# Kernel tuning notes

Measured on AMD Instinct MI355X. Metric: run time of the kernel, lower is better.

Reference implementation:

```python
import jax, jax.numpy as jnp
import numpy as np

HEAD_DIM = 64
NUM_Q_HEADS = 16
NUM_KV_HEADS = 4
MIN_TS = 1.0
MAX_TS = 10000.0


def _timescale(d):
    frac = 2.0 * jnp.arange(d // 2, dtype=jnp.float32) / d
    return MIN_TS * (MAX_TS / MIN_TS) ** frac  # [d/2]


def _rope(v, pos):
    # v: [B,S,H,D] float, pos: [B,S] int
    ts = _timescale(v.shape[-1])
    sinu = pos[:, :, None, None].astype(jnp.float32) / ts  # [B,S,1,D/2]
    sin, cos = jnp.sin(sinu), jnp.cos(sinu)
    x1, x2 = jnp.split(v.astype(jnp.float32), 2, axis=-1)
    return jnp.concatenate([x1 * cos - x2 * sin, x2 * cos + x1 * sin], axis=-1)


def setup_inputs() -> dict:
    key = jax.random.key(0)
    ks = jax.random.split(key, 5)
    B, S, E = 2, 2048, 1024
    Hq, Hk, D = NUM_Q_HEADS, NUM_KV_HEADS, HEAD_DIM
    sc = 0.02
    x = jax.random.normal(ks[0], (B, S, E), dtype=jnp.float32)
    q_pos = jnp.broadcast_to(jnp.arange(S, dtype=jnp.int32), (B, S))
    Wq = jax.random.normal(ks[1], (E, Hq * D), dtype=jnp.float32) * sc
    Wk = jax.random.normal(ks[2], (E, Hk * D), dtype=jnp.float32) * sc
    Wv = jax.random.normal(ks[3], (E, Hk * D), dtype=jnp.float32) * sc
    Wo = jax.random.normal(ks[4], (Hq * D, E), dtype=jnp.float32) * sc
    return {"x": x, "q_pos": q_pos, "Wq": Wq, "Wk": Wk, "Wv": Wv, "Wo": Wo}


def reference(x, q_pos, Wq, Wk, Wv, Wo):
    B, S, E = x.shape
    Hq, Hk, D = NUM_Q_HEADS, NUM_KV_HEADS, HEAD_DIM
    G = Hq // Hk  # gqa groups

    q = (x @ Wq).reshape(B, S, Hq, D)
    k = (x @ Wk).reshape(B, S, Hk, D)
    v = (x @ Wv).reshape(B, S, Hk, D)

    q = _rope(q, q_pos)  # kv_pos defaults to q_pos
    k = _rope(k, q_pos)

    # [B,Hk,G,S,D] grouped query heads vs shared kv heads
    qg = q.transpose(0, 2, 1, 3).reshape(B, Hk, G, S, D)
    kt = k.transpose(0, 2, 1, 3)  # [B,Hk,S,D]
    vt = v.transpose(0, 2, 1, 3)

    # NOTE: original uses scale=1.0 (no 1/sqrt(D))
    scores = jnp.einsum('bhgqd,bhkd->bhgqk', qg, kt)
    probs = jax.nn.softmax(scores, axis=-1)
    out = jnp.einsum('bhgqk,bhkd->bhgqd', probs, vt)  # [B,Hk,G,S,D]
    out = out.reshape(B, Hq, S, D).transpose(0, 2, 1, 3).reshape(B, S, Hq * D)
    return out @ Wo
```

## Files before the change

### kernel.cpp

```cpp
#include <hip/hip_runtime.h>
#include <hip/hip_fp16.h>
#include <math.h>

typedef __attribute__((ext_vector_type(8))) _Float16 half8;
typedef __attribute__((ext_vector_type(4))) _Float16 half4;
typedef __attribute__((ext_vector_type(4))) float f32x4;
typedef __attribute__((ext_vector_type(16))) float f32x16;
typedef __attribute__((ext_vector_type(4))) unsigned uint4v;

#define HQ 16
#define HK 4
#define DH 64
#define NB 2
#define SEQ 2048
#define EDIM 1024
#define KD 1024

__device__ __forceinline__ void gload16(const void* g, void* l) {
  __builtin_amdgcn_global_load_lds(
      (const __attribute__((address_space(1))) void*)g,
      (__attribute__((address_space(3))) void*)l, 16, 0, 0);
}

__global__ __launch_bounds__(256) void prep_cvt_rope(
    const float* __restrict__ x, _Float16* __restrict__ xh,
    const int* __restrict__ qpos, float2* __restrict__ tab) {
  int bx = blockIdx.x;
  int tid = threadIdx.x;
  if (bx < 4096) {
    int i = bx * 256 + tid;
    float4 v = ((const float4*)x)[i];
    half4 h;
    h[0] = (_Float16)v.x; h[1] = (_Float16)v.y; h[2] = (_Float16)v.z; h[3] = (_Float16)v.w;
    *(half4*)(xh + (size_t)i * 4) = h;
  } else {
    int i = (bx - 4096) * 256 + tid;
    int row = i >> 5, d = i & 31;
    float ang = (float)qpos[row] * expf((float)d * -0.2878231366242558f);
    float sn, cs;
    sincosf(ang, &sn, &cs);
    tab[i] = make_float2(sn, cs);
  }
}

__global__ __launch_bounds__(256) void transpose_w4(
    const float* __restrict__ Wq, const float* __restrict__ Wk,
    const float* __restrict__ Wv, const float* __restrict__ Wo,
    _Float16* __restrict__ WT, _Float16* __restrict__ WoT) {
  int z = blockIdx.z;
  const float* W;
  _Float16* dst;
  int N, roff;
  if (z == 0)      { W = Wq; N = 1024; roff = 0;    dst = WT; }
  else if (z == 1) { W = Wk; N = 256;  roff = 1024; dst = WT;  if (blockIdx.x >= 4) return; }
  else if (z == 2) { W = Wv; N = 256;  roff = 1280; dst = WT;  if (blockIdx.x >= 4) return; }
  else             { W = Wo; N = 1024; roff = 0;    dst = WoT; }

  __shared__ float t[64][65];
  int n0 = blockIdx.x * 64, k0 = blockIdx.y * 64;
  int tid = threadIdx.x;
#pragma unroll
  for (int p = 0; p < 4; ++p) {
    int idx = tid + p * 256;
    int r = idx >> 4;
    int c4 = idx & 15;
    float4 v = *(const float4*)(W + (size_t)(k0 + r) * N + n0 + c4 * 4);
    t[r][c4 * 4 + 0] = v.x; t[r][c4 * 4 + 1] = v.y;
    t[r][c4 * 4 + 2] = v.z; t[r][c4 * 4 + 3] = v.w;
  }
  __syncthreads();
#pragma unroll
  for (int p = 0; p < 4; ++p) {
    int idx = tid + p * 256;
    int n = idx >> 4;
    int k4 = idx & 15;
    half4 h;
    h[0] = (_Float16)t[k4 * 4 + 0][n]; h[1] = (_Float16)t[k4 * 4 + 1][n];
    h[2] = (_Float16)t[k4 * 4 + 2][n]; h[3] = (_Float16)t[k4 * 4 + 3][n];
    *(half4*)(dst + (size_t)(roff + n0 + n) * KD + k0 + k4 * 4) = h;
  }
}

__global__ __launch_bounds__(256) void transpose_v_kernel(const _Float16* __restrict__ vhp,
                                                          _Float16* __restrict__ vtp) {
  __shared__ _Float16 t[64][72];
  int bh = blockIdx.y;
  int s0 = blockIdx.x * 64;
  const _Float16* src = vhp + ((size_t)bh * SEQ + s0) * DH;
  _Float16* dst = vtp + (size_t)bh * DH * SEQ + s0;
  int tid = threadIdx.x;
#pragma unroll
  for (int p = 0; p < 2; ++p) {
    int idx = tid + p * 256;
    int r = idx >> 3, c8 = idx & 7;
    half8 v = *(const half8*)(src + (size_t)r * DH + c8 * 8);
#pragma unroll
    for (int i = 0; i < 8; ++i) t[r][c8 * 8 + i] = v[i];
  }
  __syncthreads();
#pragma unroll
  for (int p = 0; p < 2; ++p) {
    int idx = tid + p * 256;
    int d = idx >> 3, c8 = idx & 7;
    half8 v;
#pragma unroll
    for (int i = 0; i < 8; ++i) v[i] = t[c8 * 8 + i][d];
    *(half8*)(dst + (size_t)d * SEQ + c8 * 8) = v;
  }
}

#define SWZ(r, kb) ((kb) ^ (((r) & 7) << 4))

__global__ __launch_bounds__(256) void gemm_qkv_rope(
    const _Float16* __restrict__ xh, const _Float16* __restrict__ WT,
    const float2* __restrict__ rtab,
    _Float16* __restrict__ qh, _Float16* __restrict__ kh, _Float16* __restrict__ vh) {
  __shared__ char As[64 * 64 * 2];
  __shared__ char Bs[128 * 64 * 2];
  int tid = threadIdx.x, lane = tid & 63, wid = tid >> 6;
  int wr = wid >> 1, wc = wid & 1;
  int bm = blockIdx.x, bn = blockIdx.y;

  const char* Ag = (const char*)(xh + (size_t)bm * 64 * KD);
  const char* Bg = (const char*)(WT + (size_t)bn * 128 * KD);

  int colS = 16 * ((lane & 7) ^ (lane >> 3));
  int rS = (lane >> 3);

  f32x4 acc[2][4] = {};

  for (int kt = 0; kt < KD / 64; ++kt) {
#pragma unroll
    for (int p = 0; p < 2; ++p) {
      int sb = wid * 2 + p;
      int r = sb * 8 + rS;
      gload16(Ag + (size_t)r * (KD * 2) + kt * 128 + colS, As + sb * 1024);
    }
#pragma unroll
    for (int p = 0; p < 4; ++p) {
      int sb = wid * 4 + p;
      int r = sb * 8 + rS;
      gload16(Bg + (size_t)r * (KD * 2) + kt * 128 + colS, Bs + sb * 1024);
    }
    __syncthreads();
#pragma unroll
    for (int kk = 0; kk < 2; ++kk) {
      int kb = kk * 64 + (lane >> 4) * 16;
      half8 af[2], bf[4];
#pragma unroll
      for (int mf = 0; mf < 2; ++mf) {
        int r = wr * 32 + mf * 16 + (lane & 15);
        af[mf] = *(const half8*)(As + r * 128 + SWZ(r, kb));
      }
#pragma unroll
      for (int nf = 0; nf < 4; ++nf) {
        int r = wc * 64 + nf * 16 + (lane & 15);
        bf[nf] = *(const half8*)(Bs + r * 128 + SWZ(r, kb));
      }
#pragma unroll
      for (int mf = 0; mf < 2; ++mf)
#pragma unroll
        for (int nf = 0; nf < 4; ++nf)
          acc[mf][nf] = __builtin_amdgcn_mfma_f32_16x16x32_f16(af[mf], bf[nf], acc[mf][nf], 0, 0, 0);
    }
    __syncthreads();
  }

  int col0 = bn * 128 + wc * 64;
  int row_base = bm * 64 + wr * 32;
#pragma unroll
  for (int mf = 0; mf < 2; ++mf) {
#pragma unroll
    for (int j = 0; j < 4; ++j) {
      int row = row_base + mf * 16 + (lane >> 4) * 4 + j;
      int b = row >> 11, s = row & (SEQ - 1);
      if (col0 < 1024) {
        int hq = col0 >> 6;
        size_t base = (((size_t)b * HQ + hq) * SEQ + s) * DH;
#pragma unroll
        for (int nf = 0; nf < 2; ++nf) {
          int d = nf * 16 + (lane & 15);
          float2 scv = rtab[row * 32 + d];
          float x1 = acc[mf][nf][j], x2 = acc[mf][nf + 2][j];
          qh[base + d]      = (_Float16)(x1 * scv.y - x2 * scv.x);
          qh[base + d + 32] = (_Float16)(x2 * scv.y + x1 * scv.x);
        }
      } else if (col0 < 1280) {
        int hk = (col0 - 1024) >> 6;
        size_t base = (((size_t)b * HK + hk) * SEQ + s) * DH;
#pragma unroll
        for (int nf = 0; nf < 2; ++nf) {
          int d = nf * 16 + (lane & 15);
          float2 scv = rtab[row * 32 + d];
          float x1 = acc[mf][nf][j], x2 = acc[mf][nf + 2][j];
          kh[base + d]      = (_Float16)(x1 * scv.y - x2 * scv.x);
          kh[base + d + 32] = (_Float16)(x2 * scv.y + x1 * scv.x);
        }
      } else {
        int hk = (col0 - 1280) >> 6;
        size_t base = (((size_t)b * HK + hk) * SEQ + s) * DH;
#pragma unroll
        for (int nf = 0; nf < 4; ++nf) {
          int d = nf * 16 + (lane & 15);
          vh[base + d] = (_Float16)acc[mf][nf][j];
        }
      }
    }
  }
}

__global__ __launch_bounds__(256) void attn_kernel(
    const _Float16* __restrict__ qh, const _Float16* __restrict__ kh,
    const _Float16* __restrict__ vt, _Float16* __restrict__ oh) {
  __shared__ char Ks[128 * 64 * 2];
  __shared__ char Vs[64 * 128 * 2];

  int tid = threadIdx.x, lane = tid & 63, wid = tid >> 6;
  int half = lane >> 5, l31 = lane & 31;
  bool lopart = (half == 0);
  int qt = blockIdx.x, bh = blockIdx.y;
  int b = bh >> 4, hq = bh & 15, hk = hq >> 2;

  const _Float16* Qg = qh + (((size_t)b * HQ + hq) * SEQ + qt * 128 + wid * 32 + l31) * DH;
  const char* Kg = (const char*)(kh + (((size_t)b * HK + hk) * SEQ) * DH);
  const char* Vtg = (const char*)(vt + (size_t)(b * HK + hk) * DH * SEQ);

  const _Float16 l2e = (_Float16)1.44269504f;
  half8 qf[4];
#pragma unroll
  for (int ks = 0; ks < 4; ++ks) {
    half8 q0 = *(const half8*)(Qg + ks * 16 + half * 8);
#pragma unroll
    for (int i = 0; i < 8; ++i) q0[i] = q0[i] * l2e;
    qf[ks] = q0;
  }

  int colK = 16 * ((lane & 7) ^ (lane >> 3));
  int rK = lane >> 3;

  f32x16 oacc[2] = {};
  float m = -3e38f, l = 0.f;

  for (int kt = 0; kt < SEQ / 128; ++kt) {
#pragma unroll
    for (int p = 0; p < 4; ++p) {
      int r = (wid * 4 + p) * 8 + rK;
      gload16(Kg + (size_t)(kt * 128 + r) * 128 + colK, Ks + (wid * 4 + p) * 1024);
      int d = (wid * 4 + p) * 4 + (lane >> 4);
      int colV = ((lane & 15) * 16) ^ ((d & 7) << 4);
      gload16(Vtg + (size_t)d * (SEQ * 2) + kt * 256 + colV, Vs + (wid * 4 + p) * 1024);
    }
    __syncthreads();

    f32x16 sacc[4] = {};
    __builtin_amdgcn_s_setprio(1);
#pragma unroll
    for (int b4 = 0; b4 < 4; ++b4) {
      int r = b4 * 32 + l31;
#pragma unroll
      for (int ks = 0; ks < 4; ++ks) {
        half8 kf = *(const half8*)(Ks + r * 128 + SWZ(r, ks * 32 + half * 16));
        sacc[b4] = __builtin_amdgcn_mfma_f32_32x32x16_f16(kf, qf[ks], sacc[b4], 0, 0, 0);
      }
    }
    __builtin_amdgcn_s_setprio(0);

    float pmb[4];
#pragma unroll
    for (int b4 = 0; b4 < 4; ++b4) {
      f32x16 v = sacc[b4];
      float a0 = fmaxf(v[0], v[1]),   a1 = fmaxf(v[2], v[3]);
      float a2 = fmaxf(v[4], v[5]),   a3 = fmaxf(v[6], v[7]);
      float a4 = fmaxf(v[8], v[9]),   a5 = fmaxf(v[10], v[11]);
      float a6 = fmaxf(v[12], v[13]), a7 = fmaxf(v[14], v[15]);
      float b0 = fmaxf(a0, a1), b1 = fmaxf(a2, a3);
      float b2 = fmaxf(a4, a5), b3 = fmaxf(a6, a7);
      pmb[b4] = fmaxf(fmaxf(b0, b1), fmaxf(b2, b3));
    }
    float pm = fmaxf(fmaxf(pmb[0], pmb[1]), fmaxf(pmb[2], pmb[3]));
    pm = fmaxf(pm, __shfl_xor(pm, 32, 64));
    float mnew = fmaxf(m, pm);
    float alpha = __builtin_amdgcn_exp2f(m - mnew);
    m = mnew;
    oacc[0] *= alpha;
    oacc[1] *= alpha;
    l *= alpha;
    float ps0 = 0.f, ps1 = 0.f, ps2 = 0.f, ps3 = 0.f;

#pragma unroll
    for (int b4 = 0; b4 < 4; ++b4) {
      float e[16];
#pragma unroll
      for (int r = 0; r < 4; ++r)  { e[r] = __builtin_amdgcn_exp2f(sacc[b4][r] - m);  ps0 += e[r]; }
#pragma unroll
      for (int r = 4; r < 8; ++r)  { e[r] = __builtin_amdgcn_exp2f(sacc[b4][r] - m);  ps1 += e[r]; }
#pragma unroll
      for (int r = 8; r < 12; ++r) { e[r] = __builtin_amdgcn_exp2f(sacc[b4][r] - m);  ps2 += e[r]; }
#pragma unroll
      for (int r = 12; r < 16; ++r){ e[r] = __builtin_amdgcn_exp2f(sacc[b4][r] - m);  ps3 += e[r]; }
      unsigned W0[4], W1[4];
#pragma unroll
      for (int qd = 0; qd < 4; ++qd) {
        W0[qd] = __builtin_bit_cast(unsigned, __builtin_amdgcn_cvt_pkrtz(e[4 * qd + 0], e[4 * qd + 1]));
        W1[qd] = __builtin_bit_cast(unsigned, __builtin_amdgcn_cvt_pkrtz(e[4 * qd + 2], e[4 * qd + 3]));
      }
      half8 pf[2];
#pragma unroll
      for (int s = 0; s < 2; ++s) {
        unsigned selA = lopart ? W0[2 * s + 1] : W0[2 * s];
        unsigned crA = (unsigned)__shfl_xor((int)selA, 32, 64);
        unsigned selB = lopart ? W1[2 * s + 1] : W1[2 * s];
        unsigned crB = (unsigned)__shfl_xor((int)selB, 32, 64);
        uint4v u;
        u[0] = lopart ? W0[2 * s] : crA;
        u[1] = lopart ? W1[2 * s] : crB;
        u[2] = lopart ? crA : W0[2 * s + 1];
        u[3] = lopart ? crB : W1[2 * s + 1];
        pf[s] = __builtin_bit_cast(half8, u);
      }
      __builtin_amdgcn_s_setprio(1);
#pragma unroll
      for (int s = 0; s < 2; ++s) {
        int kvb = b4 * 64 + s * 32 + half * 16;
#pragma unroll
        for (int dblk = 0; dblk < 2; ++dblk) {
          int d = dblk * 32 + l31;
          half8 vf = *(const half8*)(Vs + d * 256 + SWZ(d, kvb));
          oacc[dblk] = __builtin_amdgcn_mfma_f32_32x32x16_f16(vf, pf[s], oacc[dblk], 0, 0, 0);
        }
      }
      __builtin_amdgcn_s_setprio(0);
    }
    float ps = (ps0 + ps1) + (ps2 + ps3);
    ps += __shfl_xor(ps, 32, 64);
    l += ps;
    __syncthreads();
  }

  int s = qt * 128 + wid * 32 + l31;
  float invl = 1.f / l;
  size_t base = ((size_t)b * SEQ + s) * 1024 + hq * 64;
#pragma unroll
  for (int dblk = 0; dblk < 2; ++dblk) {
#pragma unroll
    for (int qd = 0; qd < 4; ++qd) {
      half4 o;
#pragma unroll
      for (int j = 0; j < 4; ++j) o[j] = (_Float16)(oacc[dblk][qd * 4 + j] * invl);
      *(half4*)(oh + base + dblk * 32 + qd * 8 + half * 4) = o;
    }
  }
}

__global__ __launch_bounds__(256) void gemm_out(
    const _Float16* __restrict__ ah, const _Float16* __restrict__ WoT,
    float* __restrict__ out) {
  __shared__ char As[64 * 64 * 2];
  __shared__ char Bs[128 * 64 * 2];
  int tid = threadIdx.x, lane = tid & 63, wid = tid >> 6;
  int wr = wid >> 1, wc = wid & 1;
  int bm = blockIdx.x, bn = blockIdx.y;
  const char* Ag = (const char*)(ah + (size_t)bm * 64 * KD);
  const char* Bg = (const char*)(WoT + (size_t)bn * 128 * KD);
  int colS = 16 * ((lane & 7) ^ (lane >> 3));
  int rS = (lane >> 3);
  f32x4 acc[2][4] = {};

  for (int kt = 0; kt < KD / 64; ++kt) {
#pragma unroll
    for (int p = 0; p < 2; ++p) {
      int sb = wid * 2 + p;
      int r = sb * 8 + rS;
      gload16(Ag + (size_t)r * (KD * 2) + kt * 128 + colS, As + sb * 1024);
    }
#pragma unroll
    for (int p = 0; p < 4; ++p) {
      int sb = wid * 4 + p;
      int r = sb * 8 + rS;
      gload16(Bg + (size_t)r * (KD * 2) + kt * 128 + colS, Bs + sb * 1024);
    }
    __syncthreads();
#pragma unroll
    for (int kk = 0; kk < 2; ++kk) {
      int kb = kk * 64 + (lane >> 4) * 16;
      half8 af[2], bf[4];
#pragma unroll
      for (int mf = 0; mf < 2; ++mf) {
        int r = wr * 32 + mf * 16 + (lane & 15);
        af[mf] = *(const half8*)(As + r * 128 + SWZ(r, kb));
      }
#pragma unroll
      for (int nf = 0; nf < 4; ++nf) {
        int r = wc * 64 + nf * 16 + (lane & 15);
        bf[nf] = *(const half8*)(Bs + r * 128 + SWZ(r, kb));
      }
#pragma unroll
      for (int mf = 0; mf < 2; ++mf)
#pragma unroll
        for (int nf = 0; nf < 4; ++nf)
          acc[mf][nf] = __builtin_amdgcn_mfma_f32_16x16x32_f16(af[mf], bf[nf], acc[mf][nf], 0, 0, 0);
    }
    __syncthreads();
  }

  int row0 = bm * 64 + wr * 32, col0 = bn * 128 + wc * 64;
#pragma unroll
  for (int mf = 0; mf < 2; ++mf)
#pragma unroll
    for (int j = 0; j < 4; ++j) {
      int row = row0 + mf * 16 + (lane >> 4) * 4 + j;
#pragma unroll
      for (int nf = 0; nf < 4; ++nf)
        out[(size_t)row * 1024 + col0 + nf * 16 + (lane & 15)] = acc[mf][nf][j];
    }
}

extern "C" void kernel_launch(void* const* d_in, const int* in_sizes, int n_in,
                              void* d_out, int out_size, void* d_ws, size_t ws_size,
                              hipStream_t stream) {
  const float* x  = (const float*)d_in[0];
  const int* qpos = (const int*)d_in[1];
  const float* Wq = (const float*)d_in[2];
  const float* Wk = (const float*)d_in[3];
  const float* Wv = (const float*)d_in[4];
  const float* Wo = (const float*)d_in[5];
  float* out = (float*)d_out;

  char* ws = (char*)d_ws;
  _Float16* xh  = (_Float16*)(ws);
  _Float16* WT  = (_Float16*)(ws + 8388608);
  _Float16* WoT = (_Float16*)(ws + 11534336);
  _Float16* qhp = (_Float16*)(ws + 13631488);
  _Float16* khp = (_Float16*)(ws + 22020096);
  _Float16* vhp = (_Float16*)(ws + 24117248);
  _Float16* ohp = (_Float16*)(ws + 26214400);
  float2*   rtab = (float2*)(ws + 34603008);
  _Float16* vtp = (_Float16*)(ws + 35651584);

  prep_cvt_rope<<<4608, 256, 0, stream>>>(x, xh, qpos, rtab);
  transpose_w4<<<dim3(16, 16, 4), 256, 0, stream>>>(Wq, Wk, Wv, Wo, WT, WoT);
  gemm_qkv_rope<<<dim3(64, 12), 256, 0, stream>>>(xh, WT, rtab, qhp, khp, vhp);
  transpose_v_kernel<<<dim3(32, 8), 256, 0, stream>>>(vhp, vtp);
  attn_kernel<<<dim3(16, 32), 256, 0, stream>>>(qhp, khp, vtp, ohp);
  gemm_out<<<dim3(64, 8), 256, 0, stream>>>(ohp, WoT, out);
}
```

Baseline: 110.0 us.

## Use lazy softmax rescale, MFMA row sums, and permlane32 swap in attention

The attention inner loop now rescales the running output only when some lane's new max exceeds the old max by more than 8 in log2 units, so most tiles skip the alpha multiply. The row-sum of probabilities is computed with an extra MFMA against a vector of ones instead of scalar adds plus a cross-lane shuffle. The lane-half exchange of packed probabilities uses v_permlane32_swap in place of a shuffle with selects, and the max reduction is reorganized into three-operand form. These changes cut VALU work in the softmax at the cost of one more MFMA per sub-block, and the lazy rescale lets probabilities exceed 1 before conversion to fp16, which risks precision loss or overflow.

```diff
diff --git a/kernel.cpp b/kernel.cpp
--- a/kernel.cpp
+++ b/kernel.cpp
@@ -217,7 +217,6 @@
 
   int tid = threadIdx.x, lane = tid & 63, wid = tid >> 6;
   int half = lane >> 5, l31 = lane & 31;
-  bool lopart = (half == 0);
   int qt = blockIdx.x, bh = blockIdx.y;
   int b = bh >> 4, hq = bh & 15, hk = hq >> 2;
 
@@ -234,12 +233,16 @@
     for (int i = 0; i < 8; ++i) q0[i] = q0[i] * l2e;
     qf[ks] = q0;
   }
+  half8 ones;
+#pragma unroll
+  for (int i = 0; i < 8; ++i) ones[i] = (_Float16)1.f;
 
   int colK = 16 * ((lane & 7) ^ (lane >> 3));
   int rK = lane >> 3;
 
   f32x16 oacc[2] = {};
-  float m = -3e38f, l = 0.f;
+  f32x16 psacc = {};
+  float m = -3e38f;
 
   for (int kt = 0; kt < SEQ / 128; ++kt) {
 #pragma unroll
@@ -269,35 +272,31 @@
 #pragma unroll
     for (int b4 = 0; b4 < 4; ++b4) {
       f32x16 v = sacc[b4];
-      float a0 = fmaxf(v[0], v[1]),   a1 = fmaxf(v[2], v[3]);
-      float a2 = fmaxf(v[4], v[5]),   a3 = fmaxf(v[6], v[7]);
-      float a4 = fmaxf(v[8], v[9]),   a5 = fmaxf(v[10], v[11]);
-      float a6 = fmaxf(v[12], v[13]), a7 = fmaxf(v[14], v[15]);
-      float b0 = fmaxf(a0, a1), b1 = fmaxf(a2, a3);
-      float b2 = fmaxf(a4, a5), b3 = fmaxf(a6, a7);
-      pmb[b4] = fmaxf(fmaxf(b0, b1), fmaxf(b2, b3));
+      float t0 = fmaxf(fmaxf(v[0], v[1]), v[2]);
+      float t1 = fmaxf(fmaxf(v[3], v[4]), v[5]);
+      float t2 = fmaxf(fmaxf(v[6], v[7]), v[8]);
+      float t3 = fmaxf(fmaxf(v[9], v[10]), v[11]);
+      float t4 = fmaxf(fmaxf(v[12], v[13]), v[14]);
+      float s0 = fmaxf(fmaxf(t0, t1), t2);
+      float s1 = fmaxf(fmaxf(t3, t4), v[15]);
+      pmb[b4] = fmaxf(s0, s1);
     }
     float pm = fmaxf(fmaxf(pmb[0], pmb[1]), fmaxf(pmb[2], pmb[3]));
     pm = fmaxf(pm, __shfl_xor(pm, 32, 64));
-    float mnew = fmaxf(m, pm);
-    float alpha = __builtin_amdgcn_exp2f(m - mnew);
-    m = mnew;
-    oacc[0] *= alpha;
-    oacc[1] *= alpha;
-    l *= alpha;
-    float ps0 = 0.f, ps1 = 0.f, ps2 = 0.f, ps3 = 0.f;
+    if (__any(pm > m + 8.f)) {
+      float mnew = fmaxf(m, pm);
+      float alpha = __builtin_amdgcn_exp2f(m - mnew);
+      m = mnew;
+      oacc[0] *= alpha;
+      oacc[1] *= alpha;
+      psacc *= alpha;
+    }
 
 #pragma unroll
     for (int b4 = 0; b4 < 4; ++b4) {
       float e[16];
 #pragma unroll
-      for (int r = 0; r < 4; ++r)  { e[r] = __builtin_amdgcn_exp2f(sacc[b4][r] - m);  ps0 += e[r]; }
-#pragma unroll
-      for (int r = 4; r < 8; ++r)  { e[r] = __builtin_amdgcn_exp2f(sacc[b4][r] - m);  ps1 += e[r]; }
-#pragma unroll
-      for (int r = 8; r < 12; ++r) { e[r] = __builtin_amdgcn_exp2f(sacc[b4][r] - m);  ps2 += e[r]; }
-#pragma unroll
-      for (int r = 12; r < 16; ++r){ e[r] = __builtin_amdgcn_exp2f(sacc[b4][r] - m);  ps3 += e[r]; }
+      for (int r = 0; r < 16; ++r) e[r] = __builtin_amdgcn_exp2f(sacc[b4][r] - m);
       unsigned W0[4], W1[4];
 #pragma unroll
       for (int qd = 0; qd < 4; ++qd) {
@@ -307,21 +306,22 @@
       half8 pf[2];
 #pragma unroll
       for (int s = 0; s < 2; ++s) {
-        unsigned selA = lopart ? W0[2 * s + 1] : W0[2 * s];
-        unsigned crA = (unsigned)__shfl_xor((int)selA, 32, 64);
-        unsigned selB = lopart ? W1[2 * s + 1] : W1[2 * s];
-        unsigned crB = (unsigned)__shfl_xor((int)selB, 32, 64);
+        unsigned a0 = W0[2 * s], b0 = W0[2 * s + 1];
+        unsigned a1 = W1[2 * s], b1 = W1[2 * s + 1];
+        asm("v_permlane32_swap_b32 %0, %1" : "+v"(a0), "+v"(b0));
+        asm("v_permlane32_swap_b32 %0, %1" : "+v"(a1), "+v"(b1));
         uint4v u;
-        u[0] = lopart ? W0[2 * s] : crA;
-        u[1] = lopart ? W1[2 * s] : crB;
-        u[2] = lopart ? crA : W0[2 * s + 1];
-        u[3] = lopart ? crB : W1[2 * s + 1];
+        u[0] = a0;
+        u[1] = a1;
+        u[2] = b0;
+        u[3] = b1;
         pf[s] = __builtin_bit_cast(half8, u);
       }
       __builtin_amdgcn_s_setprio(1);
 #pragma unroll
       for (int s = 0; s < 2; ++s) {
         int kvb = b4 * 64 + s * 32 + half * 16;
+        psacc = __builtin_amdgcn_mfma_f32_32x32x16_f16(ones, pf[s], psacc, 0, 0, 0);
 #pragma unroll
         for (int dblk = 0; dblk < 2; ++dblk) {
           int d = dblk * 32 + l31;
@@ -331,14 +331,11 @@
       }
       __builtin_amdgcn_s_setprio(0);
     }
-    float ps = (ps0 + ps1) + (ps2 + ps3);
-    ps += __shfl_xor(ps, 32, 64);
-    l += ps;
     __syncthreads();
   }
 
   int s = qt * 128 + wid * 32 + l31;
-  float invl = 1.f / l;
+  float invl = 1.f / psacc[0];
   size_t base = ((size_t)b * SEQ + s) * 1024 + hq * 64;
 #pragma unroll
   for (int dblk = 0; dblk < 2; ++dblk) {
```

After: 126.4 us. 1.15x slower.
